# Kernel tuning notes

Hardware: AMD Instinct MI355X
Metric: run time of the kernel (lower is better)

## Reference

```python
import jax, jax.numpy as jnp
import numpy as np

H = 16   # n_heads == n_I
D = 64   # d_q = d_k = d_v = d_r
DX = H * D
B, S = 4, 2048

def setup_inputs() -> dict:
    key = jax.random.key(0)
    ks = jax.random.split(key, 9)
    sc = 0.02
    return {
        "value": jax.random.normal(ks[0], (B, S, DX), jnp.float32),
        "key":   jax.random.normal(ks[1], (B, S, DX), jnp.float32),
        "query": jax.random.normal(ks[2], (B, S, DX), jnp.float32),
        "Wq_w": jax.random.normal(ks[3], (DX, DX), jnp.float32) * sc,
        "Wq_b": jnp.zeros((DX,), jnp.float32),
        "Wk_w": jax.random.normal(ks[4], (DX, DX), jnp.float32) * sc,
        "Wk_b": jnp.zeros((DX,), jnp.float32),
        "Wv_w": jax.random.normal(ks[5], (DX, DX), jnp.float32) * sc,
        "Wv_b": jnp.zeros((DX,), jnp.float32),
        "Wr_w": jax.random.normal(ks[6], (DX, DX), jnp.float32) * sc,
        "Wr_b": jnp.zeros((DX,), jnp.float32),
        "Wout_w": jax.random.normal(ks[7], (DX, DX), jnp.float32) * sc,
        "Wout_b": jnp.zeros((DX,), jnp.float32),
    }

def _heads(x, b, s):
    # [b, s, H*D] -> [b, H, s, D]
    return x.reshape(b, s, H, D).transpose(0, 2, 1, 3)

def reference(value, key, query, Wq_w, Wq_b, Wk_w, Wk_b, Wv_w, Wv_b,
              Wr_w, Wr_b, Wout_w, Wout_b):
    b, s, _ = query.shape
    # torch nn.Linear: y = x @ W.T + b
    Q = _heads(query @ Wq_w.T + Wq_b, b, s)   # [b,H,s,D]
    K = _heads(key   @ Wk_w.T + Wk_b, b, s)
    V = _heads(value @ Wv_w.T + Wv_b, b, s)
    R = _heads(query @ Wr_w.T + Wr_b, b, s)
    dot_scale = jnp.sqrt(jnp.float32(D))
    scores = jnp.einsum("bhid,bhjd->bhij", Q, K) / dot_scale  # [b,H,s,s]
    attn = jax.nn.softmax(scores, axis=-1)                    # dropout p=0
    out = jnp.einsum("bhij,bhjd->bhid", attn, V)              # [b,H,s,D]
    out = out * R                                             # R-gating
    out = out.transpose(0, 2, 1, 3).reshape(b, s, H * D)
    return out @ Wout_w.T + Wout_b
```

## Files before the change

### kernel.cpp

```cpp
#include <hip/hip_runtime.h>
#include <hip/hip_bf16.h>

typedef __bf16 bf16;
typedef __bf16 bf16x4 __attribute__((ext_vector_type(4)));
typedef __bf16 bf16x8 __attribute__((ext_vector_type(8)));
typedef short  s16x4  __attribute__((ext_vector_type(4)));
typedef float  f32x4  __attribute__((ext_vector_type(4)));

#define MFMA_16x16x32(a, b, c) __builtin_amdgcn_mfma_f32_16x16x32_bf16((a), (b), (c), 0, 0, 0)

__device__ __forceinline__ f32x4 MFMA16x16x16(bf16x4 a, bf16x4 b, f32x4 c) {
#if __has_builtin(__builtin_amdgcn_mfma_f32_16x16x16_bf16)
    return __builtin_amdgcn_mfma_f32_16x16x16_bf16(a, b, c, 0, 0, 0);
#else
    union U { bf16x4 h; s16x4 s; };
    U ua, ub; ua.h = a; ub.h = b;
    return __builtin_amdgcn_mfma_f32_16x16x16bf16_1k(ua.s, ub.s, c, 0, 0, 0);
#endif
}

typedef const void __attribute__((address_space(1))) gvoid;
typedef void __attribute__((address_space(3))) svoid;

__device__ __forceinline__ void async_copy16(const void* gptr, void* ldsptr) {
    __builtin_amdgcn_global_load_lds((gvoid*)gptr, (svoid*)ldsptr, 16, 0, 0);
}

__global__ void cvt3_acts(const float* __restrict__ s0, const float* __restrict__ s1,
                          const float* __restrict__ s2,
                          bf16* __restrict__ d0, bf16* __restrict__ d1, bf16* __restrict__ d2)
{
    constexpr int N4SEG = 8192 * 1024 / 4;
    int i = blockIdx.x * blockDim.x + threadIdx.x;
    const int stride = gridDim.x * blockDim.x;
    for (; i < 3 * N4SEG; i += stride) {
        const int seg = i / N4SEG;
        const int j = i - seg * N4SEG;
        const float* s = seg == 0 ? s0 : (seg == 1 ? s1 : s2);
        bf16* d = seg == 0 ? d0 : (seg == 1 ? d1 : d2);
        float4 v = ((const float4*)s)[j];
        bf16x4 o = { (bf16)v.x, (bf16)v.y, (bf16)v.z, (bf16)v.w };
        ((bf16x4*)d)[j] = o;
    }
}

__global__ void cvt5_wts(const float* __restrict__ s0, const float* __restrict__ s1,
                         const float* __restrict__ s2, const float* __restrict__ s3,
                         const float* __restrict__ s4,
                         bf16* __restrict__ d0, bf16* __restrict__ d1, bf16* __restrict__ d2,
                         bf16* __restrict__ d3, bf16* __restrict__ d4)
{
    constexpr int N4SEG = 1024 * 1024 / 4;
    int i = blockIdx.x * blockDim.x + threadIdx.x;
    const int stride = gridDim.x * blockDim.x;
    for (; i < 5 * N4SEG; i += stride) {
        const int seg = i / N4SEG;
        const int j = i - seg * N4SEG;
        const float* s = seg == 0 ? s0 : seg == 1 ? s1 : seg == 2 ? s2 : seg == 3 ? s3 : s4;
        bf16* d = seg == 0 ? d0 : seg == 1 ? d1 : seg == 2 ? d2 : seg == 3 ? d3 : d4;
        float4 v = ((const float4*)s)[j];
        bf16x4 o = { (bf16)v.x, (bf16)v.y, (bf16)v.z, (bf16)v.w };
        ((bf16x4*)d)[j] = o;
    }
}

template <typename OutT, bool TRANS>
__global__ void gemm_nt_bias(const bf16* __restrict__ X, const bf16* __restrict__ W,
                             const float* __restrict__ bias, OutT* __restrict__ Y,
                             int M, int N, int K)
{
    constexpr int SDIM = 2048;
    __shared__ alignas(16) bf16 As[128 * 32];
    __shared__ alignas(16) bf16 Bs[128 * 32];

    const int tid  = threadIdx.x;
    const int lane = tid & 63;
    const int wave = tid >> 6;
    const int wm   = wave >> 1;
    const int wn   = wave & 1;
    const int bm   = blockIdx.x * 128;
    const int bn   = blockIdx.y * 128;
    const int l15  = lane & 15;
    const int quad = lane >> 4;

    const int srow = lane >> 2;
    const int scol = (lane & 3) * 8;

    const bf16* aseg0 = X + (size_t)(bm + wave * 32 + srow) * K + scol;
    const bf16* aseg1 = X + (size_t)(bm + wave * 32 + 16 + srow) * K + scol;
    const bf16* bseg0 = W + (size_t)(bn + wave * 32 + srow) * K + scol;
    const bf16* bseg1 = W + (size_t)(bn + wave * 32 + 16 + srow) * K + scol;
    bf16* as0 = As + (wave * 2 + 0) * 512;
    bf16* as1 = As + (wave * 2 + 1) * 512;
    bf16* bs0 = Bs + (wave * 2 + 0) * 512;
    bf16* bs1 = Bs + (wave * 2 + 1) * 512;

    f32x4 acc[4][4] = {};

    for (int k0 = 0; k0 < K; k0 += 32) {
        __syncthreads();
        async_copy16(aseg0 + k0, as0);
        async_copy16(aseg1 + k0, as1);
        async_copy16(bseg0 + k0, bs0);
        async_copy16(bseg1 + k0, bs1);
        __syncthreads();

        bf16x8 af[4], bfr[4];
        #pragma unroll
        for (int i = 0; i < 4; ++i)
            af[i] = *(const bf16x8*)(As + (wm * 64 + i * 16 + l15) * 32 + quad * 8);
        #pragma unroll
        for (int j = 0; j < 4; ++j)
            bfr[j] = *(const bf16x8*)(Bs + (wn * 64 + j * 16 + l15) * 32 + quad * 8);
        #pragma unroll
        for (int i = 0; i < 4; ++i)
            #pragma unroll
            for (int j = 0; j < 4; ++j)
                acc[i][j] = MFMA_16x16x32(af[i], bfr[j], acc[i][j]);
    }

    #pragma unroll
    for (int i = 0; i < 4; ++i) {
        const int rowg = bm + wm * 64 + i * 16 + quad * 4;
        #pragma unroll
        for (int j = 0; j < 4; ++j) {
            const int colg = bn + wn * 64 + j * 16 + l15;
            const float bv = bias[colg];
            if (TRANS) {
                bf16x4 o;
                #pragma unroll
                for (int r = 0; r < 4; ++r) o[r] = (bf16)(acc[i][j][r] + bv);
                *(bf16x4*)((bf16*)Y + (size_t)(rowg >> 11) * N * SDIM
                                    + (size_t)colg * SDIM + (rowg & (SDIM - 1))) = o;
            } else {
                #pragma unroll
                for (int r = 0; r < 4; ++r)
                    Y[(size_t)(rowg + r) * N + colg] = (OutT)(acc[i][j][r] + bv);
            }
        }
    }
}

__launch_bounds__(256, 4)
__global__ void attn_fused(const bf16* __restrict__ QRp, const bf16* __restrict__ Kp,
                           const bf16* __restrict__ Vtp, bf16* __restrict__ Op)
{
    constexpr int S = 2048, DXc = 1024, QRST = 2048, Dh = 64;
    __shared__ alignas(16) bf16 KsLo[64 * 32], KsHi[64 * 32];
    __shared__ alignas(16) bf16 VtLo[64 * 32], VtHi[64 * 32];

    const int tid  = threadIdx.x;
    const int lane = tid & 63;
    const int wave = tid >> 6;
    const int qt = blockIdx.x, h = blockIdx.y, b = blockIdx.z;
    const int l15  = lane & 15;
    const int quad = lane >> 4;

    const size_t qrbase = ((size_t)b * S) * QRST + h * Dh;
    const size_t kbase  = ((size_t)b * S) * DXc + h * Dh;
    const size_t vtbase = ((size_t)(b * 16 + h) * Dh) * S;
    const size_t obase  = ((size_t)b * S) * DXc + h * Dh;

    constexpr float QSCALE = 0.125f * 1.44269504088896340736f;
    bf16x8 qf[2][2];
    #pragma unroll
    for (int mi = 0; mi < 2; ++mi) {
        const int qrow = qt * 128 + wave * 32 + mi * 16 + l15;
        const bf16* qptr = QRp + qrbase + (size_t)qrow * QRST + quad * 8;
        qf[mi][0] = *(const bf16x8*)(qptr);
        qf[mi][1] = *(const bf16x8*)(qptr + 32);
        #pragma unroll
        for (int j = 0; j < 8; ++j) {
            qf[mi][0][j] = (bf16)((float)qf[mi][0][j] * QSCALE);
            qf[mi][1][j] = (bf16)((float)qf[mi][1][j] * QSCALE);
        }
    }

    f32x4 oacc[2][4] = {};
    float lsum[2] = {0.f, 0.f};

    const int srow = lane >> 2;
    const int scol = (lane & 3) * 8;
    const bf16* kseg = Kp  + kbase  + (size_t)(16 * wave + srow) * DXc + scol;
    const bf16* vseg = Vtp + vtbase + (size_t)(16 * wave + srow) * S   + scol;
    bf16* ksl = KsLo + wave * 512;
    bf16* ksh = KsHi + wave * 512;
    bf16* vtl = VtLo + wave * 512;
    bf16* vth = VtHi + wave * 512;

    for (int kv0 = 0; kv0 < S; kv0 += 64) {
        __syncthreads();
        async_copy16(kseg + (size_t)kv0 * DXc,      ksl);
        async_copy16(kseg + (size_t)kv0 * DXc + 32, ksh);
        async_copy16(vseg + kv0,                    vtl);
        async_copy16(vseg + kv0 + 32,               vth);
        __syncthreads();

        #pragma unroll
        for (int nb = 0; nb < 4; ++nb) {
            bf16x8 kf0 = *(const bf16x8*)(KsLo + (nb * 16 + l15) * 32 + quad * 8);
            bf16x8 kf1 = *(const bf16x8*)(KsHi + (nb * 16 + l15) * 32 + quad * 8);
            const bf16* vbase = (nb < 2) ? VtLo : VtHi;
            const int vcol = (nb & 1) * 16 + quad * 4;
            bf16x4 vtf[4];
            #pragma unroll
            for (int db = 0; db < 4; ++db)
                vtf[db] = *(const bf16x4*)(vbase + (db * 16 + l15) * 32 + vcol);

            #pragma unroll
            for (int mi = 0; mi < 2; ++mi) {
                f32x4 z = {0.f, 0.f, 0.f, 0.f};
                z = MFMA_16x16x32(kf1, qf[mi][1], z);
                z = MFMA_16x16x32(kf0, qf[mi][0], z);
                bf16x4 pt;
                #pragma unroll
                for (int r = 0; r < 4; ++r) {
                    float p = __builtin_exp2f(z[r]);
                    lsum[mi] += p;
                    pt[r] = (bf16)p;
                }
                #pragma unroll
                for (int db = 0; db < 4; ++db)
                    oacc[mi][db] = MFMA16x16x16(vtf[db], pt, oacc[mi][db]);
            }
        }
    }

    #pragma unroll
    for (int mi = 0; mi < 2; ++mi) {
        lsum[mi] += __shfl_xor(lsum[mi], 16, 64);
        lsum[mi] += __shfl_xor(lsum[mi], 32, 64);
    }

    #pragma unroll
    for (int mi = 0; mi < 2; ++mi) {
        const float inv = 1.0f / lsum[mi];
        const int qrow = qt * 128 + wave * 32 + mi * 16 + l15;
        const bf16* rrow = QRp + qrbase + (size_t)qrow * QRST + 1024;
        bf16* orow = Op + obase + (size_t)qrow * DXc;
        #pragma unroll
        for (int db = 0; db < 4; ++db) {
            bf16x4 rg = *(const bf16x4*)(rrow + db * 16 + quad * 4);
            bf16x4 o;
            #pragma unroll
            for (int r = 0; r < 4; ++r)
                o[r] = (bf16)(oacc[mi][db][r] * inv * (float)rg[r]);
            *(bf16x4*)(orow + db * 16 + quad * 4) = o;
        }
    }
}

extern "C" void kernel_launch(void* const* d_in, const int* in_sizes, int n_in,
                              void* d_out, int out_size, void* d_ws, size_t ws_size,
                              hipStream_t stream)
{
    (void)in_sizes; (void)n_in; (void)out_size; (void)ws_size;
    constexpr int B = 4, S = 2048, DX = 1024, M = B * S;
    constexpr size_t MD = (size_t)M * DX;
    constexpr size_t WD = (size_t)DX * DX;

    const float* value  = (const float*)d_in[0];
    const float* keyi   = (const float*)d_in[1];
    const float* query  = (const float*)d_in[2];
    const float* Wq_w   = (const float*)d_in[3];
    const float* Wq_b   = (const float*)d_in[4];
    const float* Wk_w   = (const float*)d_in[5];
    const float* Wk_b   = (const float*)d_in[6];
    const float* Wv_w   = (const float*)d_in[7];
    const float* Wv_b   = (const float*)d_in[8];
    const float* Wr_w   = (const float*)d_in[9];
    const float* Wr_b   = (const float*)d_in[10];
    const float* Wout_w = (const float*)d_in[11];
    const float* Wout_b = (const float*)d_in[12];

    bf16* p = (bf16*)d_ws;
    bf16* xv  = p;  p += MD;
    bf16* xk  = p;  p += MD;
    bf16* xq  = p;  p += MD;
    bf16* wqr = p;  p += 2 * WD;
    bf16* wk  = p;  p += WD;
    bf16* wv  = p;  p += WD;
    bf16* wo  = p;  p += WD;
    bf16* qr  = p;  p += 2 * MD;
    bf16* kws = p;  p += MD;
    bf16* vtws= p;  p += MD;
    float* qrb = (float*)p;
    bf16* ows = xv;

    hipMemcpyAsync(qrb,      Wq_b, DX * sizeof(float), hipMemcpyDeviceToDevice, stream);
    hipMemcpyAsync(qrb + DX, Wr_b, DX * sizeof(float), hipMemcpyDeviceToDevice, stream);

    cvt3_acts<<<dim3(2048), dim3(256), 0, stream>>>(value, keyi, query, xv, xk, xq);
    cvt5_wts <<<dim3(1024), dim3(256), 0, stream>>>(Wq_w, Wr_w, Wk_w, Wv_w, Wout_w,
                                                    wqr, wqr + WD, wk, wv, wo);

    dim3 gblk(256);
    gemm_nt_bias<bf16, false><<<dim3(M / 128, 2048 / 128), gblk, 0, stream>>>(
        xq, wqr, qrb, qr, M, 2048, DX);
    gemm_nt_bias<bf16, false><<<dim3(M / 128, DX / 128), gblk, 0, stream>>>(
        xk, wk, Wk_b, kws, M, DX, DX);
    gemm_nt_bias<bf16, true ><<<dim3(M / 128, DX / 128), gblk, 0, stream>>>(
        xv, wv, Wv_b, vtws, M, DX, DX);

    attn_fused<<<dim3(S / 128, 16, B), gblk, 0, stream>>>(qr, kws, vtws, ows);

    gemm_nt_bias<float, false><<<dim3(M / 128, DX / 128), gblk, 0, stream>>>(
        ows, wo, Wout_b, (float*)d_out, M, DX, DX);
}
```

Measured before the change: 443.9 us.

## Fuse QKV projections into one launch and stage P through LDS for K=32 MFMA

The three projection GEMMs (Q/R, K, V-transposed) are merged into a single kernel with a 32-column-tile grid that picks its input and output layout from blockIdx.y. Merging them removes two launches and helps fill the GPU. In the attention kernel, the score computation is split from the PV product. Exponentiated probabilities are written to a padded LDS buffer and read back as bf16x8 fragments, so the PV product uses 16x16x32 MFMAs instead of 16x16x16 ones. This adds LDS traffic and register pressure from holding all scores for a 64-key tile.

New measurement: 397.7 us. 10.4% less time.

```diff
diff --git a/kernel.cpp b/kernel.cpp
--- a/kernel.cpp
+++ b/kernel.cpp
@@ -4,20 +4,9 @@
 typedef __bf16 bf16;
 typedef __bf16 bf16x4 __attribute__((ext_vector_type(4)));
 typedef __bf16 bf16x8 __attribute__((ext_vector_type(8)));
-typedef short  s16x4  __attribute__((ext_vector_type(4)));
 typedef float  f32x4  __attribute__((ext_vector_type(4)));
 
 #define MFMA_16x16x32(a, b, c) __builtin_amdgcn_mfma_f32_16x16x32_bf16((a), (b), (c), 0, 0, 0)
-
-__device__ __forceinline__ f32x4 MFMA16x16x16(bf16x4 a, bf16x4 b, f32x4 c) {
-#if __has_builtin(__builtin_amdgcn_mfma_f32_16x16x16_bf16)
-    return __builtin_amdgcn_mfma_f32_16x16x16_bf16(a, b, c, 0, 0, 0);
-#else
-    union U { bf16x4 h; s16x4 s; };
-    U ua, ub; ua.h = a; ub.h = b;
-    return __builtin_amdgcn_mfma_f32_16x16x16bf16_1k(ua.s, ub.s, c, 0, 0, 0);
-#endif
-}
 
 typedef const void __attribute__((address_space(1))) gvoid;
 typedef void __attribute__((address_space(3))) svoid;
@@ -64,12 +53,97 @@
     }
 }
 
-template <typename OutT, bool TRANS>
-__global__ void gemm_nt_bias(const bf16* __restrict__ X, const bf16* __restrict__ W,
-                             const float* __restrict__ bias, OutT* __restrict__ Y,
-                             int M, int N, int K)
-{
-    constexpr int SDIM = 2048;
+__global__ void proj_fused(const bf16* __restrict__ xq, const bf16* __restrict__ xk,
+                           const bf16* __restrict__ xv, const bf16* __restrict__ wall,
+                           const float* __restrict__ ball,
+                           bf16* __restrict__ qr, bf16* __restrict__ kws,
+                           bf16* __restrict__ vtws)
+{
+    constexpr int K = 1024, SDIM = 2048;
+    __shared__ alignas(16) bf16 As[128 * 32];
+    __shared__ alignas(16) bf16 Bs[128 * 32];
+
+    const int tid  = threadIdx.x;
+    const int lane = tid & 63;
+    const int wave = tid >> 6;
+    const int wm   = wave >> 1;
+    const int wn   = wave & 1;
+    const int bm   = blockIdx.x * 128;
+    const int by   = blockIdx.y;
+    const int bn   = by * 128;
+    const int l15  = lane & 15;
+    const int quad = lane >> 4;
+
+    const bf16* X = (by < 16) ? xq : (by < 24 ? xk : xv);
+
+    const int srow = lane >> 2;
+    const int scol = (lane & 3) * 8;
+
+    const bf16* aseg0 = X + (size_t)(bm + wave * 32 + srow) * K + scol;
+    const bf16* aseg1 = X + (size_t)(bm + wave * 32 + 16 + srow) * K + scol;
+    const bf16* bseg0 = wall + (size_t)(bn + wave * 32 + srow) * K + scol;
+    const bf16* bseg1 = wall + (size_t)(bn + wave * 32 + 16 + srow) * K + scol;
+    bf16* as0 = As + (wave * 2 + 0) * 512;
+    bf16* as1 = As + (wave * 2 + 1) * 512;
+    bf16* bs0 = Bs + (wave * 2 + 0) * 512;
+    bf16* bs1 = Bs + (wave * 2 + 1) * 512;
+
+    f32x4 acc[4][4] = {};
+
+    for (int k0 = 0; k0 < K; k0 += 32) {
+        __syncthreads();
+        async_copy16(aseg0 + k0, as0);
+        async_copy16(aseg1 + k0, as1);
+        async_copy16(bseg0 + k0, bs0);
+        async_copy16(bseg1 + k0, bs1);
+        __syncthreads();
+
+        bf16x8 af[4], bfr[4];
+        #pragma unroll
+        for (int i = 0; i < 4; ++i)
+            af[i] = *(const bf16x8*)(As + (wm * 64 + i * 16 + l15) * 32 + quad * 8);
+        #pragma unroll
+        for (int j = 0; j < 4; ++j)
+            bfr[j] = *(const bf16x8*)(Bs + (wn * 64 + j * 16 + l15) * 32 + quad * 8);
+        #pragma unroll
+        for (int i = 0; i < 4; ++i)
+            #pragma unroll
+            for (int j = 0; j < 4; ++j)
+                acc[i][j] = MFMA_16x16x32(af[i], bfr[j], acc[i][j]);
+    }
+
+    #pragma unroll
+    for (int i = 0; i < 4; ++i) {
+        const int rowg = bm + wm * 64 + i * 16 + quad * 4;
+        #pragma unroll
+        for (int j = 0; j < 4; ++j) {
+            const int colg = bn + wn * 64 + j * 16 + l15;
+            const float bv = ball[colg];
+            if (by < 16) {
+                #pragma unroll
+                for (int r = 0; r < 4; ++r)
+                    qr[(size_t)(rowg + r) * 2048 + colg] = (bf16)(acc[i][j][r] + bv);
+            } else if (by < 24) {
+                const int cl = colg - 2048;
+                #pragma unroll
+                for (int r = 0; r < 4; ++r)
+                    kws[(size_t)(rowg + r) * 1024 + cl] = (bf16)(acc[i][j][r] + bv);
+            } else {
+                const int d = colg - 3072;
+                bf16x4 o;
+                #pragma unroll
+                for (int r = 0; r < 4; ++r) o[r] = (bf16)(acc[i][j][r] + bv);
+                *(bf16x4*)(vtws + (size_t)(rowg >> 11) * 1024 * SDIM
+                                + (size_t)d * SDIM + (rowg & (SDIM - 1))) = o;
+            }
+        }
+    }
+}
+
+__global__ void gemm_out(const bf16* __restrict__ X, const bf16* __restrict__ W,
+                         const float* __restrict__ bias, float* __restrict__ Y)
+{
+    constexpr int K = 1024, N = 1024;
     __shared__ alignas(16) bf16 As[128 * 32];
     __shared__ alignas(16) bf16 Bs[128 * 32];
 
@@ -126,17 +200,9 @@
         for (int j = 0; j < 4; ++j) {
             const int colg = bn + wn * 64 + j * 16 + l15;
             const float bv = bias[colg];
-            if (TRANS) {
-                bf16x4 o;
-                #pragma unroll
-                for (int r = 0; r < 4; ++r) o[r] = (bf16)(acc[i][j][r] + bv);
-                *(bf16x4*)((bf16*)Y + (size_t)(rowg >> 11) * N * SDIM
-                                    + (size_t)colg * SDIM + (rowg & (SDIM - 1))) = o;
-            } else {
-                #pragma unroll
-                for (int r = 0; r < 4; ++r)
-                    Y[(size_t)(rowg + r) * N + colg] = (OutT)(acc[i][j][r] + bv);
-            }
+            #pragma unroll
+            for (int r = 0; r < 4; ++r)
+                Y[(size_t)(rowg + r) * N + colg] = acc[i][j][r] + bv;
         }
     }
 }
@@ -146,8 +212,10 @@
                            const bf16* __restrict__ Vtp, bf16* __restrict__ Op)
 {
     constexpr int S = 2048, DXc = 1024, QRST = 2048, Dh = 64;
+    constexpr int PST = 40;
     __shared__ alignas(16) bf16 KsLo[64 * 32], KsHi[64 * 32];
     __shared__ alignas(16) bf16 VtLo[64 * 32], VtHi[64 * 32];
+    __shared__ alignas(16) bf16 Pt[4][2][2][16 * PST];
 
     const int tid  = threadIdx.x;
     const int lane = tid & 63;
@@ -196,32 +264,48 @@
         async_copy16(vseg + kv0 + 32,               vth);
         __syncthreads();
 
+        f32x4 st[2][4];
         #pragma unroll
         for (int nb = 0; nb < 4; ++nb) {
             bf16x8 kf0 = *(const bf16x8*)(KsLo + (nb * 16 + l15) * 32 + quad * 8);
             bf16x8 kf1 = *(const bf16x8*)(KsHi + (nb * 16 + l15) * 32 + quad * 8);
-            const bf16* vbase = (nb < 2) ? VtLo : VtHi;
-            const int vcol = (nb & 1) * 16 + quad * 4;
-            bf16x4 vtf[4];
-            #pragma unroll
-            for (int db = 0; db < 4; ++db)
-                vtf[db] = *(const bf16x4*)(vbase + (db * 16 + l15) * 32 + vcol);
-
             #pragma unroll
             for (int mi = 0; mi < 2; ++mi) {
                 f32x4 z = {0.f, 0.f, 0.f, 0.f};
                 z = MFMA_16x16x32(kf1, qf[mi][1], z);
-                z = MFMA_16x16x32(kf0, qf[mi][0], z);
+                st[mi][nb] = MFMA_16x16x32(kf0, qf[mi][0], z);
+            }
+        }
+        #pragma unroll
+        for (int mi = 0; mi < 2; ++mi) {
+            #pragma unroll
+            for (int nb = 0; nb < 4; ++nb) {
                 bf16x4 pt;
                 #pragma unroll
                 for (int r = 0; r < 4; ++r) {
-                    float p = __builtin_exp2f(z[r]);
+                    float p = __builtin_exp2f(st[mi][nb][r]);
                     lsum[mi] += p;
                     pt[r] = (bf16)p;
                 }
+                *(bf16x4*)(&Pt[wave][mi][nb >> 1][0] + l15 * PST
+                           + (nb & 1) * 16 + quad * 4) = pt;
+            }
+        }
+
+        #pragma unroll
+        for (int half = 0; half < 2; ++half) {
+            const bf16* vb = half ? VtHi : VtLo;
+            bf16x8 vtf[4];
+            #pragma unroll
+            for (int db = 0; db < 4; ++db)
+                vtf[db] = *(const bf16x8*)(vb + (db * 16 + l15) * 32 + quad * 8);
+            #pragma unroll
+            for (int mi = 0; mi < 2; ++mi) {
+                bf16x8 pf = *(const bf16x8*)(&Pt[wave][mi][half][0]
+                                             + l15 * PST + quad * 8);
                 #pragma unroll
                 for (int db = 0; db < 4; ++db)
-                    oacc[mi][db] = MFMA16x16x16(vtf[db], pt, oacc[mi][db]);
+                    oacc[mi][db] = MFMA_16x16x32(vtf[db], pf, oacc[mi][db]);
             }
         }
     }
@@ -274,36 +358,32 @@
     const float* Wout_b = (const float*)d_in[12];
 
     bf16* p = (bf16*)d_ws;
-    bf16* xv  = p;  p += MD;
-    bf16* xk  = p;  p += MD;
-    bf16* xq  = p;  p += MD;
-    bf16* wqr = p;  p += 2 * WD;
-    bf16* wk  = p;  p += WD;
-    bf16* wv  = p;  p += WD;
-    bf16* wo  = p;  p += WD;
-    bf16* qr  = p;  p += 2 * MD;
-    bf16* kws = p;  p += MD;
-    bf16* vtws= p;  p += MD;
-    float* qrb = (float*)p;
+    bf16* xv   = p;  p += MD;
+    bf16* xk   = p;  p += MD;
+    bf16* xq   = p;  p += MD;
+    bf16* wall = p;  p += 4 * WD;
+    bf16* wo   = p;  p += WD;
+    bf16* qr   = p;  p += 2 * MD;
+    bf16* kws  = p;  p += MD;
+    bf16* vtws = p;  p += MD;
+    float* ball = (float*)p;
     bf16* ows = xv;
 
-    hipMemcpyAsync(qrb,      Wq_b, DX * sizeof(float), hipMemcpyDeviceToDevice, stream);
-    hipMemcpyAsync(qrb + DX, Wr_b, DX * sizeof(float), hipMemcpyDeviceToDevice, stream);
+    hipMemcpyAsync(ball,            Wq_b, DX * sizeof(float), hipMemcpyDeviceToDevice, stream);
+    hipMemcpyAsync(ball + DX,       Wr_b, DX * sizeof(float), hipMemcpyDeviceToDevice, stream);
+    hipMemcpyAsync(ball + 2 * DX,   Wk_b, DX * sizeof(float), hipMemcpyDeviceToDevice, stream);
+    hipMemcpyAsync(ball + 3 * DX,   Wv_b, DX * sizeof(float), hipMemcpyDeviceToDevice, stream);
 
     cvt3_acts<<<dim3(2048), dim3(256), 0, stream>>>(value, keyi, query, xv, xk, xq);
     cvt5_wts <<<dim3(1024), dim3(256), 0, stream>>>(Wq_w, Wr_w, Wk_w, Wv_w, Wout_w,
-                                                    wqr, wqr + WD, wk, wv, wo);
-
-    dim3 gblk(256);
-    gemm_nt_bias<bf16, false><<<dim3(M / 128, 2048 / 128), gblk, 0, stream>>>(
-        xq, wqr, qrb, qr, M, 2048, DX);
-    gemm_nt_bias<bf16, false><<<dim3(M / 128, DX / 128), gblk, 0, stream>>>(
-        xk, wk, Wk_b, kws, M, DX, DX);
-    gemm_nt_bias<bf16, true ><<<dim3(M / 128, DX / 128), gblk, 0, stream>>>(
-        xv, wv, Wv_b, vtws, M, DX, DX);
-
-    attn_fused<<<dim3(S / 128, 16, B), gblk, 0, stream>>>(qr, kws, vtws, ows);
-
-    gemm_nt_bias<float, false><<<dim3(M / 128, DX / 128), gblk, 0, stream>>>(
-        ows, wo, Wout_b, (float*)d_out, M, DX, DX);
-}
+                                                    wall, wall + WD, wall + 2 * WD,
+                                                    wall + 3 * WD, wo);
+
+    proj_fused<<<dim3(M / 128, 32), dim3(256), 0, stream>>>(
+        xq, xk, xv, wall, ball, qr, kws, vtws);
+
+    attn_fused<<<dim3(S / 128, 16, B), dim3(256), 0, stream>>>(qr, kws, vtws, ows);
+
+    gemm_out<<<dim3(M / 128, DX / 128), dim3(256), 0, stream>>>(
+        ows, wo, Wout_b, (float*)d_out);
+}
```
